# Performance work log

Measured on AMD Instinct MI355X. Metric: run time of the kernel, lower is better.

Reference implementation:

```python
import jax, jax.numpy as jnp
import numpy as np

EPS = 1e-05
POOL = 10  # pooling_kernel

def setup_inputs() -> dict:
    key = jax.random.key(0)
    x = jax.random.normal(key, (8, 16, 2000, 128), dtype=jnp.float32)
    return {"x": x}

def reference(x) -> jnp.ndarray:
    B, C, T, F = x.shape
    # (B, C, T, F) -> (B, C*F, T), matching permute(0,1,3,2).reshape
    xr = jnp.transpose(x, (0, 1, 3, 2)).reshape(B, C * F, T)
    T1 = T // POOL
    # pooled block means of x and x^2 (AvgPool1d kernel=stride=POOL)
    blocks = xr[:, :, : T1 * POOL].reshape(B, C * F, T1, POOL)
    pm = blocks.mean(-1)            # (B, CF, T1)
    pm2 = (blocks ** 2).mean(-1)    # (B, CF, T1)
    # causal cumulative mean over pooled blocks (replaces O(T1^2) mask-multiply)
    nfrms = jnp.arange(1, T1 + 1, dtype=xr.dtype)  # (T1,)
    cmean = jnp.cumsum(pm, axis=-1) / nfrms
    cmean2 = jnp.cumsum(pm2, axis=-1) / nfrms
    var = cmean2 - cmean ** 2
    # repeat each block stat POOL times along time
    mean_t = jnp.repeat(cmean, POOL, axis=-1)  # (B, CF, T1*POOL)
    var_t = jnp.repeat(var, POOL, axis=-1)
    if T1 * POOL < T:  # pad tail with last stat (static branch)
        pad = T - T1 * POOL
        mean_t = jnp.concatenate([mean_t, jnp.repeat(mean_t[:, :, -1:], pad, axis=-1)], axis=-1)
        var_t = jnp.concatenate([var_t, jnp.repeat(var_t[:, :, -1:], pad, axis=-1)], axis=-1)
    x_norm = (xr - mean_t) / jnp.sqrt(var_t + EPS)
    # (B, CF, T) -> (B, C, F, T) -> (B, C, T, F)
    return jnp.transpose(x_norm.reshape(B, C, F, T), (0, 1, 3, 2))
```

## Files before the change

kernel.cpp:

```cpp
#include <hip/hip_runtime.h>

#define B_    8
#define C_    16
#define T_    2000
#define F_    128
#define F4_   32
#define POOL_ 10
#define T1_   200
#define BC_   128
#define EPS_  1e-5f

#define G_      8
#define NCHUNK_ 25
#define HF4_    16

__global__ __launch_bounds__(256) void fused_cumnorm(
    const float4* __restrict__ x4, float4* __restrict__ out4)
{
    const int tid  = (int)threadIdx.x;
    const int bc   = (int)blockIdx.x >> 1;
    const int half = (int)blockIdx.x & 1;
    const int g    = tid >> 5;
    const int k2   = (tid >> 4) & 1;
    const int f4   = tid & 15;

    __shared__ float4 sS  [G_][HF4_];
    __shared__ float4 sS2 [G_][HF4_];
    __shared__ float4 runS [2][HF4_];
    __shared__ float4 runS2[2][HF4_];

    const size_t tbase = (size_t)bc * T_ * F4_ + (size_t)half * HF4_ + (size_t)f4
                       + (size_t)(g * POOL_ + k2) * F4_;
    const float4* __restrict__ pc = x4   + tbase;
    float4*       __restrict__ qc = out4 + tbase;

    const int RS = 2 * F4_;
    const int CS = G_ * POOL_ * F4_;

    float4 v0 = pc[0], v1 = pc[RS], v2 = pc[2*RS], v3 = pc[3*RS], v4 = pc[4*RS];

    if (tid < HF4_) {
        runS [0][tid] = make_float4(0.f, 0.f, 0.f, 0.f);
        runS2[0][tid] = make_float4(0.f, 0.f, 0.f, 0.f);
    }

    for (int c = 0; c < NCHUNK_; ++c) {
        float4 s, s2;
        s.x = ((v0.x + v1.x) + (v2.x + v3.x)) + v4.x;
        s.y = ((v0.y + v1.y) + (v2.y + v3.y)) + v4.y;
        s.z = ((v0.z + v1.z) + (v2.z + v3.z)) + v4.z;
        s.w = ((v0.w + v1.w) + (v2.w + v3.w)) + v4.w;
        s2.x = v0.x*v0.x; s2.x = fmaf(v1.x,v1.x,s2.x); s2.x = fmaf(v2.x,v2.x,s2.x); s2.x = fmaf(v3.x,v3.x,s2.x); s2.x = fmaf(v4.x,v4.x,s2.x);
        s2.y = v0.y*v0.y; s2.y = fmaf(v1.y,v1.y,s2.y); s2.y = fmaf(v2.y,v2.y,s2.y); s2.y = fmaf(v3.y,v3.y,s2.y); s2.y = fmaf(v4.y,v4.y,s2.y);
        s2.z = v0.z*v0.z; s2.z = fmaf(v1.z,v1.z,s2.z); s2.z = fmaf(v2.z,v2.z,s2.z); s2.z = fmaf(v3.z,v3.z,s2.z); s2.z = fmaf(v4.z,v4.z,s2.z);
        s2.w = v0.w*v0.w; s2.w = fmaf(v1.w,v1.w,s2.w); s2.w = fmaf(v2.w,v2.w,s2.w); s2.w = fmaf(v3.w,v3.w,s2.w); s2.w = fmaf(v4.w,v4.w,s2.w);

        s.x  += __shfl_xor(s.x , 16);
        s.y  += __shfl_xor(s.y , 16);
        s.z  += __shfl_xor(s.z , 16);
        s.w  += __shfl_xor(s.w , 16);
        s2.x += __shfl_xor(s2.x, 16);
        s2.y += __shfl_xor(s2.y, 16);
        s2.z += __shfl_xor(s2.z, 16);
        s2.w += __shfl_xor(s2.w, 16);

        float4 w0, w1, w2, w3, w4;
        if (c + 1 < NCHUNK_) {
            const float4* pn = pc + CS;
            w0 = pn[0]; w1 = pn[RS]; w2 = pn[2*RS]; w3 = pn[3*RS]; w4 = pn[4*RS];
        } else {
            w0 = v0; w1 = v1; w2 = v2; w3 = v3; w4 = v4;
        }

        if (k2 == 0) { sS[g][f4] = s; sS2[g][f4] = s2; }
        __syncthreads();

        float4 acc  = runS [c & 1][f4];
        float4 acc2 = runS2[c & 1][f4];
#pragma unroll
        for (int j = 0; j < G_; ++j) {
            float4 aj  = sS [j][f4];
            float4 a2j = sS2[j][f4];
            if (j <= g) {
                acc.x  += aj.x;  acc.y  += aj.y;  acc.z  += aj.z;  acc.w  += aj.w;
                acc2.x += a2j.x; acc2.y += a2j.y; acc2.z += a2j.z; acc2.w += a2j.w;
            }
        }

        const float inv = 1.0f / (float)((c * G_ + g + 1) * POOL_);
        float4 mean, rstd;
        mean.x = acc.x * inv; rstd.x = rsqrtf(fmaf(-mean.x, mean.x, acc2.x * inv) + EPS_);
        mean.y = acc.y * inv; rstd.y = rsqrtf(fmaf(-mean.y, mean.y, acc2.y * inv) + EPS_);
        mean.z = acc.z * inv; rstd.z = rsqrtf(fmaf(-mean.z, mean.z, acc2.z * inv) + EPS_);
        mean.w = acc.w * inv; rstd.w = rsqrtf(fmaf(-mean.w, mean.w, acc2.w * inv) + EPS_);

        float4 o;
        o.x = (v0.x - mean.x) * rstd.x; o.y = (v0.y - mean.y) * rstd.y;
        o.z = (v0.z - mean.z) * rstd.z; o.w = (v0.w - mean.w) * rstd.w;
        qc[0] = o;
        o.x = (v1.x - mean.x) * rstd.x; o.y = (v1.y - mean.y) * rstd.y;
        o.z = (v1.z - mean.z) * rstd.z; o.w = (v1.w - mean.w) * rstd.w;
        qc[RS] = o;
        o.x = (v2.x - mean.x) * rstd.x; o.y = (v2.y - mean.y) * rstd.y;
        o.z = (v2.z - mean.z) * rstd.z; o.w = (v2.w - mean.w) * rstd.w;
        qc[2*RS] = o;
        o.x = (v3.x - mean.x) * rstd.x; o.y = (v3.y - mean.y) * rstd.y;
        o.z = (v3.z - mean.z) * rstd.z; o.w = (v3.w - mean.w) * rstd.w;
        qc[3*RS] = o;
        o.x = (v4.x - mean.x) * rstd.x; o.y = (v4.y - mean.y) * rstd.y;
        o.z = (v4.z - mean.z) * rstd.z; o.w = (v4.w - mean.w) * rstd.w;
        qc[4*RS] = o;

        if (g == G_ - 1 && k2 == 0) {
            runS [(c + 1) & 1][f4] = acc;
            runS2[(c + 1) & 1][f4] = acc2;
        }
        __syncthreads();

        v0 = w0; v1 = w1; v2 = w2; v3 = w3; v4 = w4;
        pc += CS; qc += CS;
    }
}

extern "C" void kernel_launch(void* const* d_in, const int* in_sizes, int n_in,
                              void* d_out, int out_size, void* d_ws, size_t ws_size,
                              hipStream_t stream)
{
    (void)in_sizes; (void)n_in; (void)d_ws; (void)ws_size; (void)out_size;
    fused_cumnorm<<<BC_ * 2, 256, 0, stream>>>(
        (const float4*)d_in[0], (float4*)d_out);
}
```

Measured before the change: 229.8 us.

## Split feature dim into quarters, widen time groups, double-buffer shared scan to drop barrier

Each (b,c) row is now split across four blocks, each covering 8 float4 feature columns, instead of two blocks of 16. Each block has 320 threads and handles 20 pooled groups per chunk, so there are 10 chunks instead of 25. The grid grows from 256 to 512 blocks, giving more parallelism on a GPU with many CUs. The shared partial sums are double-buffered by chunk parity, which allows the second __syncthreads per iteration to be removed. The prefix loop now runs a variable-length j<=g loop instead of an unrolled predicated one. Each row fetches 128 bytes, so memory transactions are narrower, and the per-thread scan gets longer.

```diff
diff --git a/kernel.cpp b/kernel.cpp
--- a/kernel.cpp
+++ b/kernel.cpp
@@ -10,27 +10,27 @@
 #define BC_   128
 #define EPS_  1e-5f
 
-#define G_      8
-#define NCHUNK_ 25
-#define HF4_    16
+#define G_      20
+#define NCHUNK_ 10
+#define QF4_    8
 
-__global__ __launch_bounds__(256) void fused_cumnorm(
+__global__ __launch_bounds__(320) void fused_cumnorm(
     const float4* __restrict__ x4, float4* __restrict__ out4)
 {
-    const int tid  = (int)threadIdx.x;
-    const int bc   = (int)blockIdx.x >> 1;
-    const int half = (int)blockIdx.x & 1;
-    const int g    = tid >> 5;
-    const int k2   = (tid >> 4) & 1;
-    const int f4   = tid & 15;
+    const int tid = (int)threadIdx.x;
+    const int bc  = (int)blockIdx.x >> 2;
+    const int q   = (int)blockIdx.x & 3;
+    const int g   = tid >> 4;
+    const int kp  = (tid >> 3) & 1;
+    const int f4  = tid & 7;
 
-    __shared__ float4 sS  [G_][HF4_];
-    __shared__ float4 sS2 [G_][HF4_];
-    __shared__ float4 runS [2][HF4_];
-    __shared__ float4 runS2[2][HF4_];
+    __shared__ float4 sS  [2][G_][QF4_];
+    __shared__ float4 sS2 [2][G_][QF4_];
+    __shared__ float4 runS [2][QF4_];
+    __shared__ float4 runS2[2][QF4_];
 
-    const size_t tbase = (size_t)bc * T_ * F4_ + (size_t)half * HF4_ + (size_t)f4
-                       + (size_t)(g * POOL_ + k2) * F4_;
+    const size_t tbase = (size_t)bc * T_ * F4_ + (size_t)(g * POOL_ + kp) * F4_
+                       + (size_t)q * QF4_ + (size_t)f4;
     const float4* __restrict__ pc = x4   + tbase;
     float4*       __restrict__ qc = out4 + tbase;
 
@@ -39,12 +39,14 @@
 
     float4 v0 = pc[0], v1 = pc[RS], v2 = pc[2*RS], v3 = pc[3*RS], v4 = pc[4*RS];
 
-    if (tid < HF4_) {
+    if (tid < QF4_) {
         runS [0][tid] = make_float4(0.f, 0.f, 0.f, 0.f);
         runS2[0][tid] = make_float4(0.f, 0.f, 0.f, 0.f);
     }
 
     for (int c = 0; c < NCHUNK_; ++c) {
+        const int p = c & 1;
+
         float4 s, s2;
         s.x = ((v0.x + v1.x) + (v2.x + v3.x)) + v4.x;
         s.y = ((v0.y + v1.y) + (v2.y + v3.y)) + v4.y;
@@ -55,14 +57,14 @@
         s2.z = v0.z*v0.z; s2.z = fmaf(v1.z,v1.z,s2.z); s2.z = fmaf(v2.z,v2.z,s2.z); s2.z = fmaf(v3.z,v3.z,s2.z); s2.z = fmaf(v4.z,v4.z,s2.z);
         s2.w = v0.w*v0.w; s2.w = fmaf(v1.w,v1.w,s2.w); s2.w = fmaf(v2.w,v2.w,s2.w); s2.w = fmaf(v3.w,v3.w,s2.w); s2.w = fmaf(v4.w,v4.w,s2.w);
 
-        s.x  += __shfl_xor(s.x , 16);
-        s.y  += __shfl_xor(s.y , 16);
-        s.z  += __shfl_xor(s.z , 16);
-        s.w  += __shfl_xor(s.w , 16);
-        s2.x += __shfl_xor(s2.x, 16);
-        s2.y += __shfl_xor(s2.y, 16);
-        s2.z += __shfl_xor(s2.z, 16);
-        s2.w += __shfl_xor(s2.w, 16);
+        s.x  += __shfl_xor(s.x , 8);
+        s.y  += __shfl_xor(s.y , 8);
+        s.z  += __shfl_xor(s.z , 8);
+        s.w  += __shfl_xor(s.w , 8);
+        s2.x += __shfl_xor(s2.x, 8);
+        s2.y += __shfl_xor(s2.y, 8);
+        s2.z += __shfl_xor(s2.z, 8);
+        s2.w += __shfl_xor(s2.w, 8);
 
         float4 w0, w1, w2, w3, w4;
         if (c + 1 < NCHUNK_) {
@@ -72,19 +74,16 @@
             w0 = v0; w1 = v1; w2 = v2; w3 = v3; w4 = v4;
         }
 
-        if (k2 == 0) { sS[g][f4] = s; sS2[g][f4] = s2; }
+        if (kp == 0) { sS[p][g][f4] = s; sS2[p][g][f4] = s2; }
         __syncthreads();
 
-        float4 acc  = runS [c & 1][f4];
-        float4 acc2 = runS2[c & 1][f4];
-#pragma unroll
-        for (int j = 0; j < G_; ++j) {
-            float4 aj  = sS [j][f4];
-            float4 a2j = sS2[j][f4];
-            if (j <= g) {
-                acc.x  += aj.x;  acc.y  += aj.y;  acc.z  += aj.z;  acc.w  += aj.w;
-                acc2.x += a2j.x; acc2.y += a2j.y; acc2.z += a2j.z; acc2.w += a2j.w;
-            }
+        float4 acc  = runS [p][f4];
+        float4 acc2 = runS2[p][f4];
+        for (int j = 0; j <= g; ++j) {
+            float4 aj  = sS [p][j][f4];
+            float4 a2j = sS2[p][j][f4];
+            acc.x  += aj.x;  acc.y  += aj.y;  acc.z  += aj.z;  acc.w  += aj.w;
+            acc2.x += a2j.x; acc2.y += a2j.y; acc2.z += a2j.z; acc2.w += a2j.w;
         }
 
         const float inv = 1.0f / (float)((c * G_ + g + 1) * POOL_);
@@ -111,11 +110,10 @@
         o.z = (v4.z - mean.z) * rstd.z; o.w = (v4.w - mean.w) * rstd.w;
         qc[4*RS] = o;
 
-        if (g == G_ - 1 && k2 == 0) {
-            runS [(c + 1) & 1][f4] = acc;
-            runS2[(c + 1) & 1][f4] = acc2;
+        if (g == G_ - 1 && kp == 0) {
+            runS [p ^ 1][f4] = acc;
+            runS2[p ^ 1][f4] = acc2;
         }
-        __syncthreads();
 
         v0 = w0; v1 = w1; v2 = w2; v3 = w3; v4 = w4;
         pc += CS; qc += CS;
@@ -127,6 +125,6 @@
                               hipStream_t stream)
 {
     (void)in_sizes; (void)n_in; (void)d_ws; (void)ws_size; (void)out_size;
-    fused_cumnorm<<<BC_ * 2, 256, 0, stream>>>(
+    fused_cumnorm<<<BC_ * 4, 320, 0, stream>>>(
         (const float4*)d_in[0], (float4*)d_out);
 }
```

After: 234.2 us. No clear change (+1.9%).
